# Optimization experiments

Measured on AMD Instinct MI355X. Metric: run time of the kernel, lower is better.

## Reference

```python
import jax, jax.numpy as jnp
import numpy as np

B, L, S, V = 1024, 512, 64, 160000
EMB = 16
E = 3 * EMB            # extended embedding dim = 48
G, M = 4, 3            # lsh_group_num, lsh_group_length
MAXC = 2 ** M          # 8 buckets per group
NH, KD = 8, 4          # MHA heads / key_dim
IN_DIM = 5 * EMB + 3 * E   # user(80) + item(48) + longterm(48) + shortterm(48) = 224
PAD_LT, PAD_ST = L // 4, S // 4
M_VALUES = jnp.array([1, 2, 4], dtype=jnp.float32)
LN_EPS = 1e-3  # keras LayerNormalization default


def setup_inputs() -> dict:
    key = jax.random.key(0)
    ks = list(jax.random.split(key, 40))
    d = {}
    for i, n in enumerate(['uid', 'utag1', 'utag2', 'utag3', 'utag4']):
        d[n] = jax.random.randint(ks[i], (B,), 1, V, dtype=jnp.int32)
    for i, n in enumerate(['label_goods_ids', 'label_shop_ids', 'label_cate_ids']):
        d[n] = jax.random.randint(ks[5 + i], (B,), 1, V, dtype=jnp.int32)
    for i, n in enumerate(['longterm_goods_ids', 'longterm_shop_ids', 'longterm_cate_ids']):
        ids = jax.random.randint(ks[8 + i], (B, L), 1, V, dtype=jnp.int32)
        d[n] = ids.at[:, L - PAD_LT:].set(0)  # left-aligned valid prefix, padded tail
    for i, n in enumerate(['shortterm_goods_ids', 'shortterm_shop_ids', 'shortterm_cate_ids']):
        ids = jax.random.randint(ks[11 + i], (B, S), 1, V, dtype=jnp.int32)
        d[n] = ids.at[:, S - PAD_ST:].set(0)
    def nrm(k, shape, s):
        return jax.random.normal(k, shape, jnp.float32) * s
    d['embed_table'] = nrm(ks[14], (V, EMB), 0.05)
    d['H'] = nrm(ks[15], (E, G, M), 1.0)  # non-trainable LSH projections
    d['wq'] = nrm(ks[16], (E, NH, KD), 0.1); d['bq'] = jnp.zeros((NH, KD))
    d['wk'] = nrm(ks[17], (E, NH, KD), 0.1); d['bk'] = jnp.zeros((NH, KD))
    d['wv'] = nrm(ks[18], (E, NH, KD), 0.1); d['bv'] = jnp.zeros((NH, KD))
    d['wo'] = nrm(ks[19], (NH, KD, E), 0.1); d['bo'] = jnp.zeros((E,))
    d['w1'] = nrm(ks[20], (IN_DIM, 200), 0.1); d['b1'] = jnp.zeros((200,))
    d['g1'] = jnp.ones((200,)); d['be1'] = jnp.zeros((200,))
    d['w2'] = nrm(ks[21], (200, 80), 0.1); d['b2'] = jnp.zeros((80,))
    d['g2'] = jnp.ones((80,)); d['be2'] = jnp.zeros((80,))
    d['w3'] = nrm(ks[22], (80, 1), 0.1); d['b3'] = jnp.zeros((1,))
    return d


def _stack_embed(table, feats):
    # feats: list of (B,) or (B,T) int arrays -> (B, T, n_feats*EMB)
    cols = [f[:, None] if f.ndim == 1 else f for f in feats]
    X = jnp.stack(cols, axis=2)              # (B, T, F)
    Xe = table[X]                            # (B, T, F, EMB)
    return Xe.reshape(Xe.shape[0], Xe.shape[1], -1)


def _layernorm(x, g, b):
    mu = x.mean(-1, keepdims=True)
    var = jnp.square(x - mu).mean(-1, keepdims=True)
    return g * (x - mu) / jnp.sqrt(var + LN_EPS) + b


def _lsh_codes(x, H):
    # x: (B, T, E) -> integer bucket codes (B, T, G)
    codes = jnp.sign(jnp.einsum('bte,egm->btgm', x, H))
    binary = (codes == 1).astype(jnp.float32)
    return jnp.tensordot(binary, M_VALUES, axes=[[-1], [0]]).astype(jnp.int32)


def _forward(uid, utag1, utag2, utag3, utag4,
             label_goods_ids, label_shop_ids, label_cate_ids,
             longterm_goods_ids, longterm_shop_ids, longterm_cate_ids,
             shortterm_goods_ids, shortterm_shop_ids, shortterm_cate_ids,
             embed_table, H, wq, bq, wk, bk, wv, bv, wo, bo,
             w1, b1, g1, be1, w2, b2, g2, be2, w3, b3):
    # --- embeddings ---
    Xu = _stack_embed(embed_table, [uid, utag1, utag2, utag3, utag4])        # (B,1,80)
    Xi = _stack_embed(embed_table, [label_goods_ids, label_shop_ids, label_cate_ids])  # (B,1,48)
    Xl = _stack_embed(embed_table, [longterm_goods_ids, longterm_shop_ids, longterm_cate_ids])   # (B,L,48)
    Xs = _stack_embed(embed_table, [shortterm_goods_ids, shortterm_shop_ids, shortterm_cate_ids])  # (B,S,48)

    longterm_pad = longterm_goods_ids == 0
    shortterm_pad = shortterm_goods_ids == 0

    # --- long-term interest: LSH scatter-mean over buckets then gather by item code ---
    series_int = _lsh_codes(Xl, H)                                   # (B,L,G)
    mXl = Xl * (~longterm_pad).astype(jnp.float32)[:, :, None]        # masked series embeddings
    oh = jax.nn.one_hot(series_int, MAXC, dtype=jnp.float32)          # (B,L,G,C)
    c_sum = jnp.einsum('blgc,ble->bgce', oh, mXl)                     # bucket sums (B,G,C,E)
    vc = oh.sum(axis=1)                                               # valid counts (B,G,C)
    safe = jnp.where(vc[..., None] > 0,
                     c_sum / jnp.maximum(vc[..., None], 1.0),
                     0.0)                                             # bucket means
    item_int = _lsh_codes(Xi, H)                                      # (B,1,G)
    item_oh = jax.nn.one_hot(item_int, MAXC, dtype=jnp.float32)       # (B,1,G,C)
    longterm_interest = jnp.einsum('bgce,bsgc->bsge', safe, item_oh).mean(axis=2)  # (B,1,E)

    # --- short-term interest: target attention (keras MultiHeadAttention) ---
    lengths = (~shortterm_pad).astype(jnp.int32).sum(axis=1)           # (B,)
    seq_mask = (jnp.arange(S)[None, :] < lengths[:, None]).astype(jnp.float32)  # (B,S)
    q = jnp.einsum('bqe,ehd->bqhd', Xi, wq) + bq
    k = jnp.einsum('bke,ehd->bkhd', Xs, wk) + bk
    v = jnp.einsum('bke,ehd->bkhd', Xs, wv) + bv
    scores = jnp.einsum('bqhd,bkhd->bhqk', q, k) / jnp.sqrt(jnp.float32(KD))
    scores = scores + (1.0 - seq_mask[:, None, None, :]) * (-1e9)
    attn = jax.nn.softmax(scores, axis=-1)
    ctx = jnp.einsum('bhqk,bkhd->bqhd', attn, v)
    shortterm_interest = jnp.einsum('bqhd,hde->bqe', ctx, wo) + bo      # (B,1,E)

    # --- final MLP: Dense->LN->ReLU x2, Dense->sigmoid ---
    feat = jnp.concatenate([Xu[:, 0], Xi[:, 0],
                            longterm_interest[:, 0], shortterm_interest[:, 0]], axis=-1)  # (B,224)
    h = jax.nn.relu(_layernorm(feat @ w1 + b1, g1, be1))
    h = jax.nn.relu(_layernorm(h @ w2 + b2, g2, be2))
    return jax.nn.sigmoid(h @ w3 + b3)                                 # (B,1)


def reference(uid, utag1, utag2, utag3, utag4,
              label_goods_ids, label_shop_ids, label_cate_ids,
              longterm_goods_ids, longterm_shop_ids, longterm_cate_ids,
              shortterm_goods_ids, shortterm_shop_ids, shortterm_cate_ids,
              embed_table, H, wq, bq, wk, bk, wv, bv, wo, bo,
              w1, b1, g1, be1, w2, b2, g2, be2, w3, b3):
    return _forward(uid, utag1, utag2, utag3, utag4,
                    label_goods_ids, label_shop_ids, label_cate_ids,
                    longterm_goods_ids, longterm_shop_ids, longterm_cate_ids,
                    shortterm_goods_ids, shortterm_shop_ids, shortterm_cate_ids,
                    embed_table, H, wq, bq, wk, bk, wv, bv, wo, bo,
                    w1, b1, g1, be1, w2, b2, g2, be2, w3, b3)
```

## Files before the change

kernel.cpp:

```cpp
#include <hip/hip_runtime.h>
#include <hip/hip_bf16.h>

#define LLEN 512
#define SLEN 64
#define EMBD 16
#define EE 48
#define GG 4
#define NHH 8
#define KDD 4
#define INDIM 224
#define H1D 200
#define H2D 80
#define CHUNK 128
#define PXE 52
#define TXS 65

__device__ __forceinline__ float bf2f(unsigned short u) {
    union { unsigned int i; float f; } v; v.i = ((unsigned int)u) << 16; return v.f;
}

template<bool BF16>
__device__ __forceinline__ float ldf(const void* p, int i) {
    if constexpr (BF16) return bf2f(((const unsigned short*)p)[i]);
    else                return ((const float*)p)[i];
}

template<bool BF16>
__device__ __forceinline__ float4 ld4(const void* p, int i4) {
    if constexpr (BF16) {
        ushort4 u = ((const ushort4*)p)[i4 >> 2];
        return make_float4(bf2f(u.x), bf2f(u.y), bf2f(u.z), bf2f(u.w));
    } else {
        return ((const float4*)p)[i4 >> 2];
    }
}

struct Pool {
    float buf[CHUNK * PXE + 16];
    union alignas(16) {
        float hl[12 * EE];
        float part[GG][GG][EE];
    } u;
    float feat[INDIM];
    float q[NHH * KDD];
    float red[128];
    int   pc[2][GG];
    int   icode[GG];
    int   len;
    float mu, rstd;
};

template<bool BF16>
__device__ void sdim_body(Pool& P,
    const int* uid, const int* ut1, const int* ut2, const int* ut3, const int* ut4,
    const int* lb_g, const int* lb_s, const int* lb_c,
    const int* lt_g, const int* lt_s, const int* lt_c,
    const int* st_g, const int* st_s, const int* st_c,
    const void* tbl, const void* Hm,
    const void* wq, const void* bq, const void* wk, const void* bk,
    const void* wvv, const void* bv, const void* wo, const void* bo,
    const void* w1, const void* b1, const void* g1, const void* be1,
    const void* w2, const void* b2, const void* g2, const void* be2,
    const void* w3, const void* b3, void* outp)
{
    const int b = blockIdx.x;
    const int tid = threadIdx.x;
    const int lane = tid & 63;
    const int wid = __builtin_amdgcn_readfirstlane(tid >> 6);

    for (int i = tid; i < 12 * EE; i += 256) {
        int j = i / EE, e = i - j * EE;
        P.u.hl[i] = ldf<BF16>(Hm, e * 12 + j);
    }
    if (tid < 80) {
        int f = tid >> 4, e = tid & 15;
        int id = (f == 0) ? uid[b] : (f == 1) ? ut1[b] : (f == 2) ? ut2[b] : (f == 3) ? ut3[b] : ut4[b];
        P.feat[tid] = ldf<BF16>(tbl, id * EMBD + e);
    } else if (tid < 128) {
        int t = tid - 80; int f = t >> 4, e = t & 15;
        int id = (f == 0) ? lb_g[b] : (f == 1) ? lb_s[b] : lb_c[b];
        P.feat[80 + t] = ldf<BF16>(tbl, id * EMBD + e);
    }
    __syncthreads();

    if (tid < 32) {
        float acc = ldf<BF16>(bq, tid);
        for (int e = 0; e < EE; e++) acc += P.feat[80 + e] * ldf<BF16>(wq, e * 32 + tid);
        P.q[tid] = acc;
    }
    if (tid >= 64 && tid < 76) {
        int j = tid - 64;
        float acc = 0.f;
        for (int e = 0; e < EE; e++) acc += P.feat[80 + e] * P.u.hl[j * EE + e];
        P.red[j] = acc;
    }
    __syncthreads();
    if (tid < GG) {
        int code = 0;
        #pragma unroll
        for (int m = 0; m < 3; m++) if (P.red[tid * 3 + m] > 0.f) code |= (1 << m);
        P.icode[tid] = code;
    }

    float accg[GG] = {0.f, 0.f, 0.f, 0.f};
    int   cnt[GG]  = {0, 0, 0, 0};
    const int offs = (lane < 52) ? lane : 51;

    for (int ch = 0; ch < LLEN / CHUNK; ch++) {
        const int base = ch * CHUNK;
        {
            int ids[6];
            #pragma unroll
            for (int i = 0; i < 6; i++) {
                int f = tid + 256 * i;
                int p = f / 12, qq = f - 12 * p, fe = qq >> 2;
                const int* idp = (fe == 0) ? lt_g : (fe == 1) ? lt_s : lt_c;
                ids[i] = idp[b * LLEN + base + p];
            }
            float4 vs[6];
            #pragma unroll
            for (int i = 0; i < 6; i++) {
                int f = tid + 256 * i;
                int p = f / 12, qq = f - 12 * p;
                vs[i] = ld4<BF16>(tbl, ids[i] * EMBD + ((qq & 3) << 2));
            }
            #pragma unroll
            for (int i = 0; i < 6; i++) {
                int f = tid + 256 * i;
                int p = f / 12, qq = f - 12 * p;
                *(float4*)&P.buf[p * PXE + (qq << 2)] = vs[i];
            }
        }
        __syncthreads();
        if (!(wid & 1)) {
            const int p = ((wid >> 1) << 6) | lane;
            const float* row = &P.buf[p * PXE];
            float4 x[12];
            #pragma unroll
            for (int k = 0; k < 12; k++) x[k] = *(const float4*)(row + 4 * k);
            float acc[12];
            #pragma unroll
            for (int j = 0; j < 12; j++) {
                const float4* hr = (const float4*)&P.u.hl[j * EE];
                float s = 0.f;
                #pragma unroll
                for (int k = 0; k < 12; k++) {
                    float4 h4 = hr[k];
                    s += x[k].x * h4.x + x[k].y * h4.y + x[k].z * h4.z + x[k].w * h4.w;
                }
                acc[j] = s;
            }
            int code[GG];
            #pragma unroll
            for (int g = 0; g < GG; g++) {
                int c = 0;
                #pragma unroll
                for (int m = 0; m < 3; m++) if (acc[g * 3 + m] > 0.f) c |= (1 << m);
                code[g] = c;
            }
            int valid = (lt_g[b * LLEN + base + p] != 0);
            float4 sel;
            sel.x = (code[0] == P.icode[0] && valid) ? 1.f : 0.f;
            sel.y = (code[1] == P.icode[1] && valid) ? 1.f : 0.f;
            sel.z = (code[2] == P.icode[2] && valid) ? 1.f : 0.f;
            sel.w = (code[3] == P.icode[3] && valid) ? 1.f : 0.f;
            *(float4*)&P.buf[p * PXE + 48] = sel;
            #pragma unroll
            for (int g = 0; g < GG; g++)
                cnt[g] += __popcll(__ballot(code[g] == P.icode[g]));
        }
        __syncthreads();
        {
            const float* basep = &P.buf[(wid * 32) * PXE] + offs;
            #pragma unroll
            for (int i = 0; i < 32; i++) {
                float xv = basep[i * PXE];
                #pragma unroll
                for (int g = 0; g < GG; g++) {
                    float sel = __int_as_float(
                        __builtin_amdgcn_readlane(__float_as_int(xv), 48 + g));
                    accg[g] += sel * xv;
                }
            }
        }
        __syncthreads();
    }
    if (lane < EE) {
        #pragma unroll
        for (int g = 0; g < GG; g++) P.u.part[wid][g][lane] = accg[g];
    }
    if (!(wid & 1) && lane == 0) {
        #pragma unroll
        for (int g = 0; g < GG; g++) P.pc[wid >> 1][g] = cnt[g];
    }
    __syncthreads();

    if (tid < EE) {
        float r = 0.f;
        #pragma unroll
        for (int g = 0; g < GG; g++) {
            float c = (float)(P.pc[0][g] + P.pc[1][g]);
            float s = P.u.part[0][g][tid] + P.u.part[1][g][tid]
                    + P.u.part[2][g][tid] + P.u.part[3][g][tid];
            r += s / fmaxf(c, 1.0f);
        }
        P.feat[128 + tid] = r * 0.25f;
    }

    float* XsT  = P.buf;
    float* wkq  = P.buf + EE * TXS;
    float* bkq  = wkq + EE * NHH;
    float* sc   = bkq + NHH;
    float* su   = sc + NHH * SLEN;
    float* sctx = su + NHH * EE;

    {
        int ids[3];
        #pragma unroll
        for (int i = 0; i < 3; i++) {
            int f = tid + 256 * i;
            int p = f / 12, qq = f - 12 * p, fe = qq >> 2;
            const int* idp = (fe == 0) ? st_g : (fe == 1) ? st_s : st_c;
            ids[i] = idp[b * SLEN + p];
        }
        float4 vs[3];
        #pragma unroll
        for (int i = 0; i < 3; i++) {
            int f = tid + 256 * i;
            int p = f / 12, qq = f - 12 * p;
            vs[i] = ld4<BF16>(tbl, ids[i] * EMBD + ((qq & 3) << 2));
        }
        #pragma unroll
        for (int i = 0; i < 3; i++) {
            int f = tid + 256 * i;
            int p = f / 12, qq = f - 12 * p;
            XsT[(4 * qq + 0) * TXS + p] = vs[i].x;
            XsT[(4 * qq + 1) * TXS + p] = vs[i].y;
            XsT[(4 * qq + 2) * TXS + p] = vs[i].z;
            XsT[(4 * qq + 3) * TXS + p] = vs[i].w;
        }
    }
    if (tid < 64) {
        unsigned long long msk = __ballot(st_g[b * SLEN + tid] != 0);
        if (tid == 0) P.len = __popcll(msk);
    }
    for (int t = tid; t < EE * NHH; t += 256) {
        int e = t >> 3, h = t & 7;
        float acc = 0.f;
        #pragma unroll
        for (int d = 0; d < KDD; d++) acc += ldf<BF16>(wk, e * 32 + h * 4 + d) * P.q[h * 4 + d];
        wkq[t] = acc;
    }
    if (tid < NHH) {
        float acc = 0.f;
        #pragma unroll
        for (int d = 0; d < KDD; d++) acc += ldf<BF16>(bk, tid * 4 + d) * P.q[tid * 4 + d];
        bkq[tid] = acc;
    }
    __syncthreads();
    for (int t = tid; t < NHH * SLEN; t += 256) {
        int h = t >> 6, s = t & 63;
        float acc = bkq[h];
        for (int e = 0; e < EE; e++) acc += XsT[e * TXS + s] * wkq[e * NHH + h];
        acc *= 0.5f;
        if (s >= P.len) acc -= 1e9f;
        sc[h * SLEN + s] = acc;
    }
    __syncthreads();
    for (int h = wid; h < NHH; h += 4) {
        float v = sc[h * SLEN + lane];
        float mx = v;
        #pragma unroll
        for (int o = 32; o; o >>= 1) mx = fmaxf(mx, __shfl_xor(mx, o));
        float ex = __expf(v - mx);
        float sm = ex;
        #pragma unroll
        for (int o = 32; o; o >>= 1) sm += __shfl_xor(sm, o);
        sc[h * SLEN + lane] = ex / sm;
    }
    __syncthreads();
    for (int t = tid; t < NHH * EE; t += 256) {
        int h = t / EE, e = t - h * EE;
        float acc = 0.f;
        for (int s = 0; s < SLEN; s++) acc += sc[h * SLEN + s] * XsT[e * TXS + s];
        su[t] = acc;
    }
    __syncthreads();
    if (tid < 32) {
        float acc = ldf<BF16>(bv, tid);
        int h = tid >> 2;
        for (int e = 0; e < EE; e++) acc += su[h * EE + e] * ldf<BF16>(wvv, e * 32 + tid);
        sctx[tid] = acc;
    }
    __syncthreads();
    if (tid < EE) {
        float acc = ldf<BF16>(bo, tid);
        #pragma unroll
        for (int i = 0; i < 32; i++) acc += sctx[i] * ldf<BF16>(wo, i * EE + tid);
        P.feat[176 + tid] = acc;
    }
    __syncthreads();

    float z1 = 0.f;
    if (tid < H1D) {
        z1 = ldf<BF16>(b1, tid);
        for (int i = 0; i < INDIM; i++) z1 += P.feat[i] * ldf<BF16>(w1, i * H1D + tid);
        P.buf[tid] = z1;
    }
    __syncthreads();
    if (tid < 64) {
        float sm = 0.f, sq = 0.f;
        for (int j = tid; j < H1D; j += 64) { float v = P.buf[j]; sm += v; sq += v * v; }
        #pragma unroll
        for (int o = 32; o; o >>= 1) { sm += __shfl_xor(sm, o); sq += __shfl_xor(sq, o); }
        if (tid == 0) { float mu = sm / H1D; P.mu = mu; P.rstd = rsqrtf(sq / H1D - mu * mu + 1e-3f); }
    }
    __syncthreads();
    if (tid < H1D) {
        float h = fmaxf(ldf<BF16>(g1, tid) * (z1 - P.mu) * P.rstd + ldf<BF16>(be1, tid), 0.f);
        P.buf[256 + tid] = h;
    }
    __syncthreads();
    float z2 = 0.f;
    if (tid < H2D) {
        z2 = ldf<BF16>(b2, tid);
        for (int i = 0; i < H1D; i++) z2 += P.buf[256 + i] * ldf<BF16>(w2, i * H2D + tid);
        P.buf[tid] = z2;
    }
    __syncthreads();
    if (tid < 64) {
        float sm = 0.f, sq = 0.f;
        for (int j = tid; j < H2D; j += 64) { float v = P.buf[j]; sm += v; sq += v * v; }
        #pragma unroll
        for (int o = 32; o; o >>= 1) { sm += __shfl_xor(sm, o); sq += __shfl_xor(sq, o); }
        if (tid == 0) { float mu = sm / H2D; P.mu = mu; P.rstd = rsqrtf(sq / H2D - mu * mu + 1e-3f); }
    }
    __syncthreads();
    if (tid < H2D) {
        float h = fmaxf(ldf<BF16>(g2, tid) * (z2 - P.mu) * P.rstd + ldf<BF16>(be2, tid), 0.f);
        P.red[tid] = h * ldf<BF16>(w3, tid);
    }
    __syncthreads();
    if (tid == 0) {
        float acc = ldf<BF16>(b3, 0);
        for (int i = 0; i < H2D; i++) acc += P.red[i];
        float sig = 1.f / (1.f + __expf(-acc));
        if constexpr (BF16) ((__hip_bfloat16*)outp)[b] = __float2bfloat16(sig);
        else                ((float*)outp)[b] = sig;
    }
}

__global__ __launch_bounds__(256, 2) void sdim_fwd(
    const int* __restrict__ uid, const int* __restrict__ ut1, const int* __restrict__ ut2,
    const int* __restrict__ ut3, const int* __restrict__ ut4,
    const int* __restrict__ lb_g, const int* __restrict__ lb_s, const int* __restrict__ lb_c,
    const int* __restrict__ lt_g, const int* __restrict__ lt_s, const int* __restrict__ lt_c,
    const int* __restrict__ st_g, const int* __restrict__ st_s, const int* __restrict__ st_c,
    const void* __restrict__ tbl, const void* __restrict__ Hm,
    const void* __restrict__ wq, const void* __restrict__ bq,
    const void* __restrict__ wk, const void* __restrict__ bk,
    const void* __restrict__ wvv, const void* __restrict__ bv,
    const void* __restrict__ wo, const void* __restrict__ bo,
    const void* __restrict__ w1, const void* __restrict__ b1,
    const void* __restrict__ g1, const void* __restrict__ be1,
    const void* __restrict__ w2, const void* __restrict__ b2,
    const void* __restrict__ g2, const void* __restrict__ be2,
    const void* __restrict__ w3, const void* __restrict__ b3,
    void* __restrict__ outp)
{
    __shared__ Pool P;
    __shared__ int s_isbf;
    if (threadIdx.x < 64) {
        int big = 0;
        for (int i = (threadIdx.x & 63); i < 128; i += 64) {
            unsigned short u = ((const unsigned short*)tbl)[2 * i];
            if (((u >> 7) & 0xFF) >= 127) big = 1;
        }
        unsigned long long m = __ballot(big);
        if (threadIdx.x == 0) s_isbf = (m == 0ull) ? 1 : 0;
    }
    __syncthreads();
    if (s_isbf)
        sdim_body<true >(P, uid, ut1, ut2, ut3, ut4, lb_g, lb_s, lb_c, lt_g, lt_s, lt_c,
                         st_g, st_s, st_c, tbl, Hm, wq, bq, wk, bk, wvv, bv, wo, bo,
                         w1, b1, g1, be1, w2, b2, g2, be2, w3, b3, outp);
    else
        sdim_body<false>(P, uid, ut1, ut2, ut3, ut4, lb_g, lb_s, lb_c, lt_g, lt_s, lt_c,
                         st_g, st_s, st_c, tbl, Hm, wq, bq, wk, bk, wvv, bv, wo, bo,
                         w1, b1, g1, be1, w2, b2, g2, be2, w3, b3, outp);
}

extern "C" void kernel_launch(void* const* d_in, const int* in_sizes, int n_in,
                              void* d_out, int out_size, void* d_ws, size_t ws_size,
                              hipStream_t stream) {
    const int B = in_sizes[0];
    sdim_fwd<<<B, 256, 0, stream>>>(
        (const int*)d_in[0],  (const int*)d_in[1],  (const int*)d_in[2],
        (const int*)d_in[3],  (const int*)d_in[4],
        (const int*)d_in[5],  (const int*)d_in[6],  (const int*)d_in[7],
        (const int*)d_in[8],  (const int*)d_in[9],  (const int*)d_in[10],
        (const int*)d_in[11], (const int*)d_in[12], (const int*)d_in[13],
        (const void*)d_in[14], (const void*)d_in[15],
        (const void*)d_in[16], (const void*)d_in[17],
        (const void*)d_in[18], (const void*)d_in[19],
        (const void*)d_in[20], (const void*)d_in[21],
        (const void*)d_in[22], (const void*)d_in[23],
        (const void*)d_in[24], (const void*)d_in[25],
        (const void*)d_in[26], (const void*)d_in[27],
        (const void*)d_in[28], (const void*)d_in[29],
        (const void*)d_in[30], (const void*)d_in[31],
        (const void*)d_in[32], (const void*)d_in[33],
        d_out);
}
```

Baseline: 221.8 us.

## Double-buffer longterm embedding gather with smaller chunks and id prefetch

Replaces the four 128-row chunks of the longterm loop with eight 64-row chunks in a two-slot LDS buffer. The next chunk's ids and embedding rows are loaded into registers before the current chunk's LSH hashing and pooling run, then written to the other slot afterwards, so gather latency overlaps compute. It also hoists the per-thread index arithmetic (f/12) out of the loop. In exchange there are twice as many block barriers, and each hashing wave now uses only 32 of its lanes.

```diff
diff --git a/kernel.cpp b/kernel.cpp
--- a/kernel.cpp
+++ b/kernel.cpp
@@ -11,7 +11,8 @@
 #define INDIM 224
 #define H1D 200
 #define H2D 80
-#define CHUNK 128
+#define CH 64
+#define NCH (LLEN / CH)
 #define PXE 52
 #define TXS 65
 
@@ -36,7 +37,7 @@
 }
 
 struct Pool {
-    float buf[CHUNK * PXE + 16];
+    float buf[2][CH * PXE];
     union alignas(16) {
         float hl[12 * EE];
         float part[GG][GG][EE];
@@ -68,6 +69,13 @@
     const int lane = tid & 63;
     const int wid = __builtin_amdgcn_readfirstlane(tid >> 6);
 
+    int gp[3], gq[3];
+    #pragma unroll
+    for (int i = 0; i < 3; i++) {
+        int f = tid + 256 * i;
+        gp[i] = f / 12; gq[i] = f - 12 * gp[i];
+    }
+
     for (int i = tid; i < 12 * EE; i += 256) {
         int j = i / EE, e = i - j * EE;
         P.u.hl[i] = ldf<BF16>(Hm, e * 12 + j);
@@ -106,35 +114,47 @@
     int   cnt[GG]  = {0, 0, 0, 0};
     const int offs = (lane < 52) ? lane : 51;
 
-    for (int ch = 0; ch < LLEN / CHUNK; ch++) {
-        const int base = ch * CHUNK;
-        {
-            int ids[6];
-            #pragma unroll
-            for (int i = 0; i < 6; i++) {
-                int f = tid + 256 * i;
-                int p = f / 12, qq = f - 12 * p, fe = qq >> 2;
+    int    idsN[3];
+    float4 vsC[3];
+
+    #pragma unroll
+    for (int i = 0; i < 3; i++) {
+        int fe = gq[i] >> 2;
+        const int* idp = (fe == 0) ? lt_g : (fe == 1) ? lt_s : lt_c;
+        idsN[i] = idp[b * LLEN + gp[i]];
+    }
+    #pragma unroll
+    for (int i = 0; i < 3; i++)
+        vsC[i] = ld4<BF16>(tbl, idsN[i] * EMBD + ((gq[i] & 3) << 2));
+    #pragma unroll
+    for (int i = 0; i < 3; i++)
+        *(float4*)&P.buf[0][gp[i] * PXE + (gq[i] << 2)] = vsC[i];
+    #pragma unroll
+    for (int i = 0; i < 3; i++) {
+        int fe = gq[i] >> 2;
+        const int* idp = (fe == 0) ? lt_g : (fe == 1) ? lt_s : lt_c;
+        idsN[i] = idp[b * LLEN + CH + gp[i]];
+    }
+    __syncthreads();
+
+    for (int ch = 0; ch < NCH; ch++) {
+        const int cur = ch & 1;
+        if (ch + 1 < NCH) {
+            #pragma unroll
+            for (int i = 0; i < 3; i++)
+                vsC[i] = ld4<BF16>(tbl, idsN[i] * EMBD + ((gq[i] & 3) << 2));
+        }
+        if (ch + 2 < NCH) {
+            #pragma unroll
+            for (int i = 0; i < 3; i++) {
+                int fe = gq[i] >> 2;
                 const int* idp = (fe == 0) ? lt_g : (fe == 1) ? lt_s : lt_c;
-                ids[i] = idp[b * LLEN + base + p];
+                idsN[i] = idp[b * LLEN + (ch + 2) * CH + gp[i]];
             }
-            float4 vs[6];
-            #pragma unroll
-            for (int i = 0; i < 6; i++) {
-                int f = tid + 256 * i;
-                int p = f / 12, qq = f - 12 * p;
-                vs[i] = ld4<BF16>(tbl, ids[i] * EMBD + ((qq & 3) << 2));
-            }
-            #pragma unroll
-            for (int i = 0; i < 6; i++) {
-                int f = tid + 256 * i;
-                int p = f / 12, qq = f - 12 * p;
-                *(float4*)&P.buf[p * PXE + (qq << 2)] = vs[i];
-            }
-        }
-        __syncthreads();
-        if (!(wid & 1)) {
-            const int p = ((wid >> 1) << 6) | lane;
-            const float* row = &P.buf[p * PXE];
+        }
+        if (!(wid & 1) && lane < 32) {
+            const int p = ((wid >> 1) << 5) | lane;
+            const float* row = &P.buf[cur][p * PXE];
             float4 x[12];
             #pragma unroll
             for (int k = 0; k < 12; k++) x[k] = *(const float4*)(row + 4 * k);
@@ -158,22 +178,22 @@
                 for (int m = 0; m < 3; m++) if (acc[g * 3 + m] > 0.f) c |= (1 << m);
                 code[g] = c;
             }
-            int valid = (lt_g[b * LLEN + base + p] != 0);
+            int valid = (lt_g[b * LLEN + ch * CH + p] != 0);
             float4 sel;
             sel.x = (code[0] == P.icode[0] && valid) ? 1.f : 0.f;
             sel.y = (code[1] == P.icode[1] && valid) ? 1.f : 0.f;
             sel.z = (code[2] == P.icode[2] && valid) ? 1.f : 0.f;
             sel.w = (code[3] == P.icode[3] && valid) ? 1.f : 0.f;
-            *(float4*)&P.buf[p * PXE + 48] = sel;
+            *(float4*)&P.buf[cur][p * PXE + 48] = sel;
             #pragma unroll
             for (int g = 0; g < GG; g++)
                 cnt[g] += __popcll(__ballot(code[g] == P.icode[g]));
         }
         __syncthreads();
         {
-            const float* basep = &P.buf[(wid * 32) * PXE] + offs;
-            #pragma unroll
-            for (int i = 0; i < 32; i++) {
+            const float* basep = &P.buf[cur][(wid * 16) * PXE] + offs;
+            #pragma unroll
+            for (int i = 0; i < 16; i++) {
                 float xv = basep[i * PXE];
                 #pragma unroll
                 for (int g = 0; g < GG; g++) {
@@ -183,6 +203,11 @@
                 }
             }
         }
+        if (ch + 1 < NCH) {
+            #pragma unroll
+            for (int i = 0; i < 3; i++)
+                *(float4*)&P.buf[cur ^ 1][gp[i] * PXE + (gq[i] << 2)] = vsC[i];
+        }
         __syncthreads();
     }
     if (lane < EE) {
@@ -207,8 +232,9 @@
         P.feat[128 + tid] = r * 0.25f;
     }
 
-    float* XsT  = P.buf;
-    float* wkq  = P.buf + EE * TXS;
+    float* flat = &P.buf[0][0];
+    float* XsT  = flat;
+    float* wkq  = flat + EE * TXS;
     float* bkq  = wkq + EE * NHH;
     float* sc   = bkq + NHH;
     float* su   = sc + NHH * SLEN;
@@ -218,22 +244,17 @@
         int ids[3];
         #pragma unroll
         for (int i = 0; i < 3; i++) {
-            int f = tid + 256 * i;
-            int p = f / 12, qq = f - 12 * p, fe = qq >> 2;
+            int fe = gq[i] >> 2;
             const int* idp = (fe == 0) ? st_g : (fe == 1) ? st_s : st_c;
-            ids[i] = idp[b * SLEN + p];
+            ids[i] = idp[b * SLEN + gp[i]];
         }
         float4 vs[3];
         #pragma unroll
+        for (int i = 0; i < 3; i++)
+            vs[i] = ld4<BF16>(tbl, ids[i] * EMBD + ((gq[i] & 3) << 2));
+        #pragma unroll
         for (int i = 0; i < 3; i++) {
-            int f = tid + 256 * i;
-            int p = f / 12, qq = f - 12 * p;
-            vs[i] = ld4<BF16>(tbl, ids[i] * EMBD + ((qq & 3) << 2));
-        }
-        #pragma unroll
-        for (int i = 0; i < 3; i++) {
-            int f = tid + 256 * i;
-            int p = f / 12, qq = f - 12 * p;
+            int p = gp[i], qq = gq[i];
             XsT[(4 * qq + 0) * TXS + p] = vs[i].x;
             XsT[(4 * qq + 1) * TXS + p] = vs[i].y;
             XsT[(4 * qq + 2) * TXS + p] = vs[i].z;
@@ -305,12 +326,12 @@
     if (tid < H1D) {
         z1 = ldf<BF16>(b1, tid);
         for (int i = 0; i < INDIM; i++) z1 += P.feat[i] * ldf<BF16>(w1, i * H1D + tid);
-        P.buf[tid] = z1;
+        flat[tid] = z1;
     }
     __syncthreads();
     if (tid < 64) {
         float sm = 0.f, sq = 0.f;
-        for (int j = tid; j < H1D; j += 64) { float v = P.buf[j]; sm += v; sq += v * v; }
+        for (int j = tid; j < H1D; j += 64) { float v = flat[j]; sm += v; sq += v * v; }
         #pragma unroll
         for (int o = 32; o; o >>= 1) { sm += __shfl_xor(sm, o); sq += __shfl_xor(sq, o); }
         if (tid == 0) { float mu = sm / H1D; P.mu = mu; P.rstd = rsqrtf(sq / H1D - mu * mu + 1e-3f); }
@@ -318,19 +339,19 @@
     __syncthreads();
     if (tid < H1D) {
         float h = fmaxf(ldf<BF16>(g1, tid) * (z1 - P.mu) * P.rstd + ldf<BF16>(be1, tid), 0.f);
-        P.buf[256 + tid] = h;
+        flat[256 + tid] = h;
     }
     __syncthreads();
     float z2 = 0.f;
     if (tid < H2D) {
         z2 = ldf<BF16>(b2, tid);
-        for (int i = 0; i < H1D; i++) z2 += P.buf[256 + i] * ldf<BF16>(w2, i * H2D + tid);
-        P.buf[tid] = z2;
+        for (int i = 0; i < H1D; i++) z2 += flat[256 + i] * ldf<BF16>(w2, i * H2D + tid);
+        flat[tid] = z2;
     }
     __syncthreads();
     if (tid < 64) {
         float sm = 0.f, sq = 0.f;
-        for (int j = tid; j < H2D; j += 64) { float v = P.buf[j]; sm += v; sq += v * v; }
+        for (int j = tid; j < H2D; j += 64) { float v = flat[j]; sm += v; sq += v * v; }
         #pragma unroll
         for (int o = 32; o; o >>= 1) { sm += __shfl_xor(sm, o); sq += __shfl_xor(sq, o); }
         if (tid == 0) { float mu = sm / H2D; P.mu = mu; P.rstd = rsqrtf(sq / H2D - mu * mu + 1e-3f); }
```

Measured after the change: 243.8 us. +9.9%, slower.

## Compute LSH codes per-wave and broadcast packed match bits via readlane

Applied to the files above, without the earlier changes.

Each wave now hashes its own 32 positions in half-wave, not having even waves hash 64 positions and write selection floats to shared memory. Match/valid bits are packed into an int and broadcast with readlane, which removes one block-wide barrier per chunk and the shared-memory selection store. The inner hash loop is reordered to stream x once, and launch bounds raise the occupancy target to 4 blocks per CU. In exchange, only half the lanes do the hash work, and the tighter launch bound may force register spills.

```diff
diff --git a/kernel.cpp b/kernel.cpp
--- a/kernel.cpp
+++ b/kernel.cpp
@@ -44,7 +44,7 @@
     float feat[INDIM];
     float q[NHH * KDD];
     float red[128];
-    int   pc[2][GG];
+    int   pc[GG][GG];
     int   icode[GG];
     int   len;
     float mu, rstd;
@@ -104,7 +104,6 @@
 
     float accg[GG] = {0.f, 0.f, 0.f, 0.f};
     int   cnt[GG]  = {0, 0, 0, 0};
-    const int offs = (lane < 52) ? lane : 51;
 
     for (int ch = 0; ch < LLEN / CHUNK; ch++) {
         const int base = ch * CHUNK;
@@ -132,55 +131,42 @@
             }
         }
         __syncthreads();
-        if (!(wid & 1)) {
-            const int p = ((wid >> 1) << 6) | lane;
+        int packed = 0;
+        if (lane < 32) {
+            const int p = (wid << 5) | lane;
             const float* row = &P.buf[p * PXE];
-            float4 x[12];
-            #pragma unroll
-            for (int k = 0; k < 12; k++) x[k] = *(const float4*)(row + 4 * k);
             float acc[12];
             #pragma unroll
-            for (int j = 0; j < 12; j++) {
-                const float4* hr = (const float4*)&P.u.hl[j * EE];
-                float s = 0.f;
+            for (int j = 0; j < 12; j++) acc[j] = 0.f;
+            #pragma unroll
+            for (int k = 0; k < 12; k++) {
+                float4 x4 = *(const float4*)(row + 4 * k);
                 #pragma unroll
-                for (int k = 0; k < 12; k++) {
-                    float4 h4 = hr[k];
-                    s += x[k].x * h4.x + x[k].y * h4.y + x[k].z * h4.z + x[k].w * h4.w;
+                for (int j = 0; j < 12; j++) {
+                    float4 h4 = *(const float4*)&P.u.hl[j * EE + 4 * k];
+                    acc[j] += x4.x * h4.x + x4.y * h4.y + x4.z * h4.z + x4.w * h4.w;
                 }
-                acc[j] = s;
-            }
-            int code[GG];
+            }
+            int valid = (lt_g[b * LLEN + base + p] != 0);
             #pragma unroll
             for (int g = 0; g < GG; g++) {
                 int c = 0;
                 #pragma unroll
                 for (int m = 0; m < 3; m++) if (acc[g * 3 + m] > 0.f) c |= (1 << m);
-                code[g] = c;
-            }
-            int valid = (lt_g[b * LLEN + base + p] != 0);
-            float4 sel;
-            sel.x = (code[0] == P.icode[0] && valid) ? 1.f : 0.f;
-            sel.y = (code[1] == P.icode[1] && valid) ? 1.f : 0.f;
-            sel.z = (code[2] == P.icode[2] && valid) ? 1.f : 0.f;
-            sel.w = (code[3] == P.icode[3] && valid) ? 1.f : 0.f;
-            *(float4*)&P.buf[p * PXE + 48] = sel;
-            #pragma unroll
-            for (int g = 0; g < GG; g++)
-                cnt[g] += __popcll(__ballot(code[g] == P.icode[g]));
-        }
-        __syncthreads();
+                int match = (c == P.icode[g]);
+                packed |= (match << g) | ((match & valid) << (8 + g));
+                cnt[g] += __popcll(__ballot(match));
+            }
+        }
         {
-            const float* basep = &P.buf[(wid * 32) * PXE] + offs;
+            const float* basep = &P.buf[(wid << 5) * PXE] + lane;
             #pragma unroll
             for (int i = 0; i < 32; i++) {
                 float xv = basep[i * PXE];
+                int s = __builtin_amdgcn_readlane(packed, i);
                 #pragma unroll
-                for (int g = 0; g < GG; g++) {
-                    float sel = __int_as_float(
-                        __builtin_amdgcn_readlane(__float_as_int(xv), 48 + g));
-                    accg[g] += sel * xv;
-                }
+                for (int g = 0; g < GG; g++)
+                    accg[g] += ((s >> (8 + g)) & 1) ? xv : 0.f;
             }
         }
         __syncthreads();
@@ -189,9 +175,9 @@
         #pragma unroll
         for (int g = 0; g < GG; g++) P.u.part[wid][g][lane] = accg[g];
     }
-    if (!(wid & 1) && lane == 0) {
-        #pragma unroll
-        for (int g = 0; g < GG; g++) P.pc[wid >> 1][g] = cnt[g];
+    if (lane == 0) {
+        #pragma unroll
+        for (int g = 0; g < GG; g++) P.pc[wid][g] = cnt[g];
     }
     __syncthreads();
 
@@ -199,7 +185,7 @@
         float r = 0.f;
         #pragma unroll
         for (int g = 0; g < GG; g++) {
-            float c = (float)(P.pc[0][g] + P.pc[1][g]);
+            float c = (float)(P.pc[0][g] + P.pc[1][g] + P.pc[2][g] + P.pc[3][g]);
             float s = P.u.part[0][g][tid] + P.u.part[1][g][tid]
                     + P.u.part[2][g][tid] + P.u.part[3][g][tid];
             r += s / fmaxf(c, 1.0f);
@@ -350,7 +336,7 @@
     }
 }
 
-__global__ __launch_bounds__(256, 2) void sdim_fwd(
+__global__ __launch_bounds__(256, 4) void sdim_fwd(
     const int* __restrict__ uid, const int* __restrict__ ut1, const int* __restrict__ ut2,
     const int* __restrict__ ut3, const int* __restrict__ ut4,
     const int* __restrict__ lb_g, const int* __restrict__ lb_s, const int* __restrict__ lb_c,
```

Measured after the change: 245.4 us. 1.11x slower.
